# Optimization experiments

Measured on AMD Instinct MI355X. Metric: run time of the kernel, lower is better.

The kernel has to match this reference:

```python
import jax, jax.numpy as jnp
import numpy as np


def _lstm_cell(x_t, h, c, w_ih, w_hh, b):
    # x_t, h, c: [B, 1]; w_ih, w_hh: [4, 1]; b: [4]
    # PyTorch gate order: input, forget, cell(g), output
    gates = x_t @ w_ih.T + h @ w_hh.T + b  # [B, 4]
    i, f, g, o = jnp.split(gates, 4, axis=-1)
    i = jax.nn.sigmoid(i)
    f = jax.nn.sigmoid(f)
    o = jax.nn.sigmoid(o)
    g = jnp.tanh(g)
    c = f * c + i * g
    h = o * jnp.tanh(c)
    return h, c


def setup_inputs() -> dict:
    key = jax.random.key(0)
    ks = jax.random.split(key, 8)
    B, T_IN, STEPS = 32768, 1024, 512
    return {
        "x": jax.random.normal(ks[0], (B, 1, T_IN), dtype=jnp.float32),
        "t": jax.random.normal(ks[1], (B, 1, STEPS), dtype=jnp.float32),
        "h0": jax.random.normal(ks[2], (B, 1), dtype=jnp.float32),
        "c0": jax.random.normal(ks[3], (B, 1), dtype=jnp.float32),
        "w_ih": jax.random.normal(ks[4], (4, 1), dtype=jnp.float32),
        "w_hh": jax.random.normal(ks[5], (4, 1), dtype=jnp.float32),
        "b_ih": jax.random.normal(ks[6], (4,), dtype=jnp.float32) * 0.1,
        "b_hh": jax.random.normal(ks[7], (4,), dtype=jnp.float32) * 0.1,
    }


def reference(x, t, h0, c0, w_ih, w_hh, b_ih, b_hh):
    b = b_ih + b_hh
    # open loop: feed every input timestep through the LSTM cell
    xs = jnp.transpose(x[:, 0, :], (1, 0))[:, :, None]  # [T_in, B, 1]

    def open_step(carry, x_t):
        h, c = carry
        h, c = _lstm_cell(x_t, h, c, w_ih, w_hh, b)
        return (h, c), None

    (h, c), _ = jax.lax.scan(open_step, (h0, c0), xs)

    ts = jnp.transpose(t[:, 0, :], (1, 0))[:, :, None]  # [steps, B, 1]

    def closed_step(carry, _):
        h, c, x_in = carry
        h, c = _lstm_cell(x_in, h, c, w_ih, w_hh, b)
        return (h, c, h), h

    steps = ts.shape[0]
    _, preds = jax.lax.scan(closed_step, (h, c, xs[-1]), None, length=steps)
    # criterion = MSELoss(mean), accumulated per step:
    # sum_t mean_B((pred_t - t_t)^2)
    loss = jnp.sum(jnp.mean((preds - ts) ** 2, axis=(1, 2)))
    # pred_seq is detached numpy in the original -> stop_gradient here
    pred_seq = jax.lax.stop_gradient(jnp.transpose(preds[:, :, 0], (1, 0)))  # [B, steps]
    return loss, pred_seq
```

## Files before the change

### kernel.cpp

```cpp
#include <hip/hip_runtime.h>


#define L2E 1.44269504088896340736f
#define B_TOT 32768
#define T_IN 1024
#define STEPS 512
#define CPB 32
#define CH 64
#define PAD 65

__device__ __forceinline__ float ex2(float x){ return __builtin_amdgcn_exp2f(x); }
__device__ __forceinline__ float rcp(float x){ return __builtin_amdgcn_rcpf(x); }
__device__ __forceinline__ float dpp_swap1(float v){
    return __int_as_float(__builtin_amdgcn_mov_dpp(__float_as_int(v), 0xB1, 0xF, 0xF, true));
}

struct LaneK { float A1,B1,C1, A2,B2,C2, W1,W2; };

__device__ __forceinline__ void finish_step(float z1, float z2, bool odd,
                                            float& h, float& C){
    float e1 = ex2(z1);
    float e2 = ex2(z2);
    float r1 = rcp(1.0f + e1);
    float r2 = rcp(1.0f + e2);
    float s1 = dpp_swap1(r1);
    float s2 = dpp_swap1(r2);
    float ri = odd ? s1 : r1;
    float rf = odd ? r1 : s1;
    float rg = odd ? s2 : r2;
    float ro = odd ? r2 : s2;
    float g2  = fmaf(rg, -4.0f * L2E, 2.0f * L2E);
    float rfC = rf * C;
    C = fmaf(ri, g2, rfC);
    float rc = rcp(1.0f + ex2(C));
    float u  = rc + rc;
    h = fmaf(-u, ro, ro);
}

__device__ __forceinline__ void stage_issue32(const float* __restrict__ base,
                                              int row_stride, int col0, int lane,
                                              float4* v){
    const int r_lo = lane >> 4, c4 = lane & 15;
    #pragma unroll
    for (int j = 0; j < 8; ++j)
        v[j] = *(const float4*)(base + (size_t)(j*4 + r_lo) * row_stride + col0 + c4*4);
}
__device__ __forceinline__ void stage_write32(float* __restrict__ lds, int lane,
                                              const float4* v){
    const int r_lo = lane >> 4, c4 = lane & 15;
    #pragma unroll
    for (int j = 0; j < 8; ++j){
        float* p = lds + (j*4 + r_lo) * PAD + c4*4;
        p[0]=v[j].x; p[1]=v[j].y; p[2]=v[j].z; p[3]=v[j].w;
    }
}

__global__ __launch_bounds__(64) void lstm_chain_kernel(
    const float* __restrict__ x, const float* __restrict__ t,
    const float* __restrict__ h0, const float* __restrict__ c0,
    const float* __restrict__ w_ih, const float* __restrict__ w_hh,
    const float* __restrict__ b_ih, const float* __restrict__ b_hh,
    float* __restrict__ out)
{
    __shared__ float sb[2][CPB * PAD];
    __shared__ float pb[CPB * PAD];

    const int lane = threadIdx.x;
    const bool odd = lane & 1;
    const int ch   = lane >> 1;
    const int b0   = blockIdx.x * CPB;

    LaneK K;
    {
        float bi = b_ih[0] + b_hh[0], bf = b_ih[1] + b_hh[1];
        float bg = b_ih[2] + b_hh[2], bo = b_ih[3] + b_hh[3];
        float Ai = -L2E*w_ih[0], Bi = -L2E*w_hh[0], Ci = -L2E*bi;
        float Af = -L2E*w_ih[1], Bf = -L2E*w_hh[1], Cf = -L2E*bf;
        float Ag = 2.0f*L2E*w_ih[2], Bg = 2.0f*L2E*w_hh[2], Cg = 2.0f*L2E*bg;
        float Ao = -L2E*w_ih[3], Bo = -L2E*w_hh[3], Co = -L2E*bo;
        K.A1 = odd ? Af : Ai;  K.B1 = odd ? Bf : Bi;  K.C1 = odd ? Cf : Ci;
        K.A2 = odd ? Ao : Ag;  K.B2 = odd ? Bo : Bg;  K.C2 = odd ? Co : Cg;
        K.W1 = K.A1 + K.B1;    K.W2 = K.A2 + K.B2;
    }

    float h = h0[b0 + ch];
    float C = (2.0f * L2E) * c0[b0 + ch];

    const float* xbase = x + (size_t)b0 * T_IN;
    const float* tbase = t + (size_t)b0 * STEPS;

    { float4 stg[8]; stage_issue32(xbase, T_IN, 0, lane, stg); stage_write32(sb[0], lane, stg); }
    #pragma unroll 1
    for (int k = 0; k < T_IN / CH; ++k){
        float4 stg[8];
        if (k < T_IN/CH - 1) stage_issue32(xbase, T_IN, (k+1)*CH, lane, stg);
        const float* xrow = &sb[k & 1][ch * PAD];
        #pragma unroll 4
        for (int s = 0; s < CH; ++s){
            float xv = xrow[s];
            float z1 = fmaf(xv, K.A1, fmaf(h, K.B1, K.C1));
            float z2 = fmaf(xv, K.A2, fmaf(h, K.B2, K.C2));
            finish_step(z1, z2, odd, h, C);
        }
        if (k < T_IN/CH - 1) stage_write32(sb[(k+1) & 1], lane, stg);
    }
    float xin = sb[(T_IN/CH - 1) & 1][ch * PAD + (CH - 1)];

    { float4 stg[8]; stage_issue32(tbase, STEPS, 0, lane, stg); stage_write32(sb[0], lane, stg); }
    float lacc = 0.0f;

    auto cstep = [&](int s, const float* trow, float* prow){
        float z1 = fmaf(h, K.W1, K.C1);
        float z2 = fmaf(h, K.W2, K.C2);
        finish_step(z1, z2, odd, h, C);
        float d = h - trow[s];
        lacc = fmaf(d, d, lacc);
        prow[s] = h;
    };

    #pragma unroll 1
    for (int k = 0; k < STEPS / CH; ++k){
        float4 stg[8];
        if (k < STEPS/CH - 1) stage_issue32(tbase, STEPS, (k+1)*CH, lane, stg);
        const float* trow = &sb[k & 1][ch * PAD];
        float* prow = &pb[ch * PAD];
        if (k == 0){
            float z1 = fmaf(xin, K.A1, fmaf(h, K.B1, K.C1));
            float z2 = fmaf(xin, K.A2, fmaf(h, K.B2, K.C2));
            finish_step(z1, z2, odd, h, C);
            float d = h - trow[0];
            lacc = fmaf(d, d, lacc);
            prow[0] = h;
            #pragma unroll 4
            for (int s = 1; s < CH; ++s) cstep(s, trow, prow);
        } else {
            #pragma unroll 4
            for (int s = 0; s < CH; ++s) cstep(s, trow, prow);
        }
        float* obase = out + 1 + (size_t)b0 * STEPS + k * CH;
        #pragma unroll 4
        for (int r = 0; r < CPB; ++r)
            obase[(size_t)r * STEPS + lane] = pb[r * PAD + lane];
        if (k < STEPS/CH - 1) stage_write32(sb[(k+1) & 1], lane, stg);
    }

    #pragma unroll
    for (int off = 32; off > 0; off >>= 1)
        lacc += __shfl_down(lacc, off, 64);
    if (lane == 0)
        atomicAdd(out, lacc * (0.5f / (float)B_TOT));
}

extern "C" void kernel_launch(void* const* d_in, const int* in_sizes, int n_in,
                              void* d_out, int out_size, void* d_ws, size_t ws_size,
                              hipStream_t stream) {
    const float* x    = (const float*)d_in[0];
    const float* t    = (const float*)d_in[1];
    const float* h0   = (const float*)d_in[2];
    const float* c0   = (const float*)d_in[3];
    const float* w_ih = (const float*)d_in[4];
    const float* w_hh = (const float*)d_in[5];
    const float* b_ih = (const float*)d_in[6];
    const float* b_hh = (const float*)d_in[7];
    float* out = (float*)d_out;

    hipMemsetAsync(out, 0, sizeof(float), stream);

    lstm_chain_kernel<<<B_TOT / CPB, 64, 0, stream>>>(
        x, t, h0, c0, w_ih, w_hh, b_ih, b_hh, out);
}
```

Baseline: 331.1 us.

## Split LSTM gates across four lanes per chain with quad DPP broadcasts

Each batch chain now uses four lanes, one per gate, where it previously used two lanes each holding two gates. Each lane does a single exp/rcp for its gate and the four gate values are broadcast within the quad through DPP quad_perm. This shortens the per-step dependent instruction chain, at the cost of halving the chains per wave and doubling the number of blocks. The input-projection FMAs are hoisted off the recurrence, staging now uses vectorized float4 LDS reads and writes, and __syncthreads barriers plus a rescaled loss factor are added to match the new lane mapping.

```diff
diff --git a/kernel.cpp b/kernel.cpp
--- a/kernel.cpp
+++ b/kernel.cpp
@@ -5,54 +5,44 @@
 #define B_TOT 32768
 #define T_IN 1024
 #define STEPS 512
-#define CPB 32
+#define CPB 16
 #define CH 64
-#define PAD 65
+#define PAD 68
 
 __device__ __forceinline__ float ex2(float x){ return __builtin_amdgcn_exp2f(x); }
 __device__ __forceinline__ float rcp(float x){ return __builtin_amdgcn_rcpf(x); }
-__device__ __forceinline__ float dpp_swap1(float v){
-    return __int_as_float(__builtin_amdgcn_mov_dpp(__float_as_int(v), 0xB1, 0xF, 0xF, true));
+
+template<int CTRL>
+__device__ __forceinline__ float qperm(float v){
+    return __int_as_float(__builtin_amdgcn_mov_dpp(__float_as_int(v), CTRL, 0xF, 0xF, true));
 }
 
-struct LaneK { float A1,B1,C1, A2,B2,C2, W1,W2; };
-
-__device__ __forceinline__ void finish_step(float z1, float z2, bool odd,
-                                            float& h, float& C){
-    float e1 = ex2(z1);
-    float e2 = ex2(z2);
-    float r1 = rcp(1.0f + e1);
-    float r2 = rcp(1.0f + e2);
-    float s1 = dpp_swap1(r1);
-    float s2 = dpp_swap1(r2);
-    float ri = odd ? s1 : r1;
-    float rf = odd ? r1 : s1;
-    float rg = odd ? s2 : r2;
-    float ro = odd ? r2 : s2;
-    float g2  = fmaf(rg, -4.0f * L2E, 2.0f * L2E);
-    float rfC = rf * C;
-    C = fmaf(ri, g2, rfC);
+__device__ __forceinline__ void lstm_tail(float z, float& h, float& C){
+    float r  = rcp(1.0f + ex2(z));
+    float ri = qperm<0x00>(r);
+    float rf = qperm<0x55>(r);
+    float rg = qperm<0xAA>(r);
+    float ro = qperm<0xFF>(r);
+    float g2 = fmaf(rg, -4.0f * L2E, 2.0f * L2E);
+    C = fmaf(rf, C, ri * g2);
     float rc = rcp(1.0f + ex2(C));
     float u  = rc + rc;
     h = fmaf(-u, ro, ro);
 }
 
-__device__ __forceinline__ void stage_issue32(const float* __restrict__ base,
-                                              int row_stride, int col0, int lane,
-                                              float4* v){
+__device__ __forceinline__ void stage_issue16(const float* __restrict__ base,
+                                              int rs, int col0, int lane, float4* v){
     const int r_lo = lane >> 4, c4 = lane & 15;
     #pragma unroll
-    for (int j = 0; j < 8; ++j)
-        v[j] = *(const float4*)(base + (size_t)(j*4 + r_lo) * row_stride + col0 + c4*4);
+    for (int j = 0; j < 4; ++j)
+        v[j] = *(const float4*)(base + (size_t)(j*4 + r_lo) * rs + col0 + c4*4);
 }
-__device__ __forceinline__ void stage_write32(float* __restrict__ lds, int lane,
+__device__ __forceinline__ void stage_write16(float* __restrict__ lds, int lane,
                                               const float4* v){
     const int r_lo = lane >> 4, c4 = lane & 15;
     #pragma unroll
-    for (int j = 0; j < 8; ++j){
-        float* p = lds + (j*4 + r_lo) * PAD + c4*4;
-        p[0]=v[j].x; p[1]=v[j].y; p[2]=v[j].z; p[3]=v[j].w;
-    }
+    for (int j = 0; j < 4; ++j)
+        *(float4*)(lds + (j*4 + r_lo) * PAD + c4*4) = v[j];
 }
 
 __global__ __launch_bounds__(64) void lstm_chain_kernel(
@@ -66,22 +56,15 @@
     __shared__ float pb[CPB * PAD];
 
     const int lane = threadIdx.x;
-    const bool odd = lane & 1;
-    const int ch   = lane >> 1;
+    const int g    = lane & 3;
+    const int ch   = lane >> 2;
     const int b0   = blockIdx.x * CPB;
 
-    LaneK K;
-    {
-        float bi = b_ih[0] + b_hh[0], bf = b_ih[1] + b_hh[1];
-        float bg = b_ih[2] + b_hh[2], bo = b_ih[3] + b_hh[3];
-        float Ai = -L2E*w_ih[0], Bi = -L2E*w_hh[0], Ci = -L2E*bi;
-        float Af = -L2E*w_ih[1], Bf = -L2E*w_hh[1], Cf = -L2E*bf;
-        float Ag = 2.0f*L2E*w_ih[2], Bg = 2.0f*L2E*w_hh[2], Cg = 2.0f*L2E*bg;
-        float Ao = -L2E*w_ih[3], Bo = -L2E*w_hh[3], Co = -L2E*bo;
-        K.A1 = odd ? Af : Ai;  K.B1 = odd ? Bf : Bi;  K.C1 = odd ? Cf : Ci;
-        K.A2 = odd ? Ao : Ag;  K.B2 = odd ? Bo : Bg;  K.C2 = odd ? Co : Cg;
-        K.W1 = K.A1 + K.B1;    K.W2 = K.A2 + K.B2;
-    }
+    float sc = (g == 2) ? (2.0f * L2E) : (-L2E);
+    float A  = sc * w_ih[g];
+    float Bh = sc * w_hh[g];
+    float Cb = sc * (b_ih[g] + b_hh[g]);
+    float W  = A + Bh;
 
     float h = h0[b0 + ch];
     float C = (2.0f * L2E) * c0[b0 + ch];
@@ -89,66 +72,68 @@
     const float* xbase = x + (size_t)b0 * T_IN;
     const float* tbase = t + (size_t)b0 * STEPS;
 
-    { float4 stg[8]; stage_issue32(xbase, T_IN, 0, lane, stg); stage_write32(sb[0], lane, stg); }
+    { float4 stg[4]; stage_issue16(xbase, T_IN, 0, lane, stg); stage_write16(sb[0], lane, stg); }
     #pragma unroll 1
     for (int k = 0; k < T_IN / CH; ++k){
-        float4 stg[8];
-        if (k < T_IN/CH - 1) stage_issue32(xbase, T_IN, (k+1)*CH, lane, stg);
-        const float* xrow = &sb[k & 1][ch * PAD];
+        float4 stg[4];
+        if (k < T_IN/CH - 1) stage_issue16(xbase, T_IN, (k+1)*CH, lane, stg);
+        __syncthreads();
+        const float4* xrow = (const float4*)(&sb[k & 1][ch * PAD]);
         #pragma unroll 4
-        for (int s = 0; s < CH; ++s){
-            float xv = xrow[s];
-            float z1 = fmaf(xv, K.A1, fmaf(h, K.B1, K.C1));
-            float z2 = fmaf(xv, K.A2, fmaf(h, K.B2, K.C2));
-            finish_step(z1, z2, odd, h, C);
+        for (int s4 = 0; s4 < CH/4; ++s4){
+            float4 xq = xrow[s4];
+            float zx0 = fmaf(xq.x, A, Cb);
+            float zx1 = fmaf(xq.y, A, Cb);
+            float zx2 = fmaf(xq.z, A, Cb);
+            float zx3 = fmaf(xq.w, A, Cb);
+            lstm_tail(fmaf(h, Bh, zx0), h, C);
+            lstm_tail(fmaf(h, Bh, zx1), h, C);
+            lstm_tail(fmaf(h, Bh, zx2), h, C);
+            lstm_tail(fmaf(h, Bh, zx3), h, C);
         }
-        if (k < T_IN/CH - 1) stage_write32(sb[(k+1) & 1], lane, stg);
+        if (k < T_IN/CH - 1) stage_write16(sb[(k+1) & 1], lane, stg);
     }
     float xin = sb[(T_IN/CH - 1) & 1][ch * PAD + (CH - 1)];
 
-    { float4 stg[8]; stage_issue32(tbase, STEPS, 0, lane, stg); stage_write32(sb[0], lane, stg); }
+    { float4 stg[4]; stage_issue16(tbase, STEPS, 0, lane, stg); stage_write16(sb[0], lane, stg); }
     float lacc = 0.0f;
-
-    auto cstep = [&](int s, const float* trow, float* prow){
-        float z1 = fmaf(h, K.W1, K.C1);
-        float z2 = fmaf(h, K.W2, K.C2);
-        finish_step(z1, z2, odd, h, C);
-        float d = h - trow[s];
-        lacc = fmaf(d, d, lacc);
-        prow[s] = h;
-    };
-
     #pragma unroll 1
     for (int k = 0; k < STEPS / CH; ++k){
-        float4 stg[8];
-        if (k < STEPS/CH - 1) stage_issue32(tbase, STEPS, (k+1)*CH, lane, stg);
-        const float* trow = &sb[k & 1][ch * PAD];
-        float* prow = &pb[ch * PAD];
-        if (k == 0){
-            float z1 = fmaf(xin, K.A1, fmaf(h, K.B1, K.C1));
-            float z2 = fmaf(xin, K.A2, fmaf(h, K.B2, K.C2));
-            finish_step(z1, z2, odd, h, C);
-            float d = h - trow[0];
-            lacc = fmaf(d, d, lacc);
-            prow[0] = h;
-            #pragma unroll 4
-            for (int s = 1; s < CH; ++s) cstep(s, trow, prow);
-        } else {
-            #pragma unroll 4
-            for (int s = 0; s < CH; ++s) cstep(s, trow, prow);
+        float4 stg[4];
+        if (k < STEPS/CH - 1) stage_issue16(tbase, STEPS, (k+1)*CH, lane, stg);
+        __syncthreads();
+        const float4* trow = (const float4*)(&sb[k & 1][ch * PAD]);
+        #pragma unroll 2
+        for (int s4 = 0; s4 < CH/4; ++s4){
+            float4 tq = trow[s4];
+            float p0, p1, p2, p3, d;
+            if (k == 0 && s4 == 0)
+                lstm_tail(fmaf(xin, A, fmaf(h, Bh, Cb)), h, C);
+            else
+                lstm_tail(fmaf(h, W, Cb), h, C);
+            p0 = h; d = h - tq.x; lacc = fmaf(d, d, lacc);
+            lstm_tail(fmaf(h, W, Cb), h, C);
+            p1 = h; d = h - tq.y; lacc = fmaf(d, d, lacc);
+            lstm_tail(fmaf(h, W, Cb), h, C);
+            p2 = h; d = h - tq.z; lacc = fmaf(d, d, lacc);
+            lstm_tail(fmaf(h, W, Cb), h, C);
+            p3 = h; d = h - tq.w; lacc = fmaf(d, d, lacc);
+            if (g == 0)
+                *(float4*)(&pb[ch * PAD + s4 * 4]) = make_float4(p0, p1, p2, p3);
         }
+        __syncthreads();
         float* obase = out + 1 + (size_t)b0 * STEPS + k * CH;
         #pragma unroll 4
         for (int r = 0; r < CPB; ++r)
             obase[(size_t)r * STEPS + lane] = pb[r * PAD + lane];
-        if (k < STEPS/CH - 1) stage_write32(sb[(k+1) & 1], lane, stg);
+        if (k < STEPS/CH - 1) stage_write16(sb[(k+1) & 1], lane, stg);
     }
 
     #pragma unroll
     for (int off = 32; off > 0; off >>= 1)
         lacc += __shfl_down(lacc, off, 64);
     if (lane == 0)
-        atomicAdd(out, lacc * (0.5f / (float)B_TOT));
+        atomicAdd(out, lacc * (0.25f / (float)B_TOT));
 }
 
 extern "C" void kernel_launch(void* const* d_in, const int* in_sizes, int n_in,
```

After: 357.0 us. 7.8% more time.

## Shorten LSTM recurrence critical path and move loss out of the step loop

Applied to the files above, without the earlier changes.

Gate exchange between lane pairs now uses quad-permute DPP broadcasts, so the per-lane odd/even selects disappear from the serial dependency chain. The cell tail is reordered so the input term is computed off the h dependency and ro*2 is ready before the final rcp. The squared-error loss accumulation moves out of the per-step loop into the coalesced output write-back pass, reading targets from LDS. Because each element is now counted once instead of twice per lane pair, the scale changes from 0.5/B to 1/B. Unroll factors are raised to 8.

```diff
diff --git a/kernel.cpp b/kernel.cpp
--- a/kernel.cpp
+++ b/kernel.cpp
@@ -11,39 +11,34 @@
 
 __device__ __forceinline__ float ex2(float x){ return __builtin_amdgcn_exp2f(x); }
 __device__ __forceinline__ float rcp(float x){ return __builtin_amdgcn_rcpf(x); }
-__device__ __forceinline__ float dpp_swap1(float v){
-    return __int_as_float(__builtin_amdgcn_mov_dpp(__float_as_int(v), 0xB1, 0xF, 0xF, true));
+template<int CTRL>
+__device__ __forceinline__ float qp(float v){
+    return __int_as_float(__builtin_amdgcn_mov_dpp(__float_as_int(v), CTRL, 0xF, 0xF, true));
 }
 
 struct LaneK { float A1,B1,C1, A2,B2,C2, W1,W2; };
 
-__device__ __forceinline__ void finish_step(float z1, float z2, bool odd,
-                                            float& h, float& C){
-    float e1 = ex2(z1);
-    float e2 = ex2(z2);
-    float r1 = rcp(1.0f + e1);
-    float r2 = rcp(1.0f + e2);
-    float s1 = dpp_swap1(r1);
-    float s2 = dpp_swap1(r2);
-    float ri = odd ? s1 : r1;
-    float rf = odd ? r1 : s1;
-    float rg = odd ? s2 : r2;
-    float ro = odd ? r2 : s2;
-    float g2  = fmaf(rg, -4.0f * L2E, 2.0f * L2E);
-    float rfC = rf * C;
-    C = fmaf(ri, g2, rfC);
-    float rc = rcp(1.0f + ex2(C));
-    float u  = rc + rc;
-    h = fmaf(-u, ro, ro);
+__device__ __forceinline__ void tail(float z1, float z2, float& h, float& C){
+    float r1 = rcp(1.0f + ex2(z1));
+    float r2 = rcp(1.0f + ex2(z2));
+    float ri = qp<0xA0>(r1);
+    float rf = qp<0xF5>(r1);
+    float rg = qp<0xA0>(r2);
+    float ro = qp<0xF5>(r2);
+    float g2 = fmaf(rg, -4.0f * L2E, 2.0f * L2E);
+    C = fmaf(rf, C, ri * g2);
+    float e   = ex2(C);
+    float ro2 = ro + ro;
+    float rc  = rcp(1.0f + e);
+    h = fmaf(-rc, ro2, ro);
 }
 
 __device__ __forceinline__ void stage_issue32(const float* __restrict__ base,
-                                              int row_stride, int col0, int lane,
-                                              float4* v){
+                                              int rs, int col0, int lane, float4* v){
     const int r_lo = lane >> 4, c4 = lane & 15;
     #pragma unroll
     for (int j = 0; j < 8; ++j)
-        v[j] = *(const float4*)(base + (size_t)(j*4 + r_lo) * row_stride + col0 + c4*4);
+        v[j] = *(const float4*)(base + (size_t)(j*4 + r_lo) * rs + col0 + c4*4);
 }
 __device__ __forceinline__ void stage_write32(float* __restrict__ lds, int lane,
                                               const float4* v){
@@ -95,52 +90,50 @@
         float4 stg[8];
         if (k < T_IN/CH - 1) stage_issue32(xbase, T_IN, (k+1)*CH, lane, stg);
         const float* xrow = &sb[k & 1][ch * PAD];
-        #pragma unroll 4
+        #pragma unroll 8
         for (int s = 0; s < CH; ++s){
             float xv = xrow[s];
-            float z1 = fmaf(xv, K.A1, fmaf(h, K.B1, K.C1));
-            float z2 = fmaf(xv, K.A2, fmaf(h, K.B2, K.C2));
-            finish_step(z1, z2, odd, h, C);
+            float z1 = fmaf(h, K.B1, fmaf(xv, K.A1, K.C1));
+            float z2 = fmaf(h, K.B2, fmaf(xv, K.A2, K.C2));
+            tail(z1, z2, h, C);
         }
         if (k < T_IN/CH - 1) stage_write32(sb[(k+1) & 1], lane, stg);
     }
-    float xin = sb[(T_IN/CH - 1) & 1][ch * PAD + (CH - 1)];
+    float xin = sb[1][ch * PAD + (CH - 1)];
 
     { float4 stg[8]; stage_issue32(tbase, STEPS, 0, lane, stg); stage_write32(sb[0], lane, stg); }
     float lacc = 0.0f;
-
-    auto cstep = [&](int s, const float* trow, float* prow){
-        float z1 = fmaf(h, K.W1, K.C1);
-        float z2 = fmaf(h, K.W2, K.C2);
-        finish_step(z1, z2, odd, h, C);
-        float d = h - trow[s];
-        lacc = fmaf(d, d, lacc);
-        prow[s] = h;
-    };
-
     #pragma unroll 1
     for (int k = 0; k < STEPS / CH; ++k){
         float4 stg[8];
         if (k < STEPS/CH - 1) stage_issue32(tbase, STEPS, (k+1)*CH, lane, stg);
-        const float* trow = &sb[k & 1][ch * PAD];
         float* prow = &pb[ch * PAD];
         if (k == 0){
-            float z1 = fmaf(xin, K.A1, fmaf(h, K.B1, K.C1));
-            float z2 = fmaf(xin, K.A2, fmaf(h, K.B2, K.C2));
-            finish_step(z1, z2, odd, h, C);
-            float d = h - trow[0];
-            lacc = fmaf(d, d, lacc);
+            tail(fmaf(h, K.B1, fmaf(xin, K.A1, K.C1)),
+                 fmaf(h, K.B2, fmaf(xin, K.A2, K.C2)), h, C);
             prow[0] = h;
-            #pragma unroll 4
-            for (int s = 1; s < CH; ++s) cstep(s, trow, prow);
+            #pragma unroll 8
+            for (int s = 1; s < CH; ++s){
+                tail(fmaf(h, K.W1, K.C1), fmaf(h, K.W2, K.C2), h, C);
+                prow[s] = h;
+            }
         } else {
-            #pragma unroll 4
-            for (int s = 0; s < CH; ++s) cstep(s, trow, prow);
+            #pragma unroll 8
+            for (int s = 0; s < CH; ++s){
+                tail(fmaf(h, K.W1, K.C1), fmaf(h, K.W2, K.C2), h, C);
+                prow[s] = h;
+            }
         }
+        const float* trow = &sb[k & 1][0];
         float* obase = out + 1 + (size_t)b0 * STEPS + k * CH;
         #pragma unroll 4
-        for (int r = 0; r < CPB; ++r)
-            obase[(size_t)r * STEPS + lane] = pb[r * PAD + lane];
+        for (int r = 0; r < CPB; ++r){
+            float p  = pb[r * PAD + lane];
+            float tv = trow[r * PAD + lane];
+            float d  = p - tv;
+            lacc = fmaf(d, d, lacc);
+            obase[(size_t)r * STEPS + lane] = p;
+        }
         if (k < STEPS/CH - 1) stage_write32(sb[(k+1) & 1], lane, stg);
     }
 
@@ -148,7 +141,7 @@
     for (int off = 32; off > 0; off >>= 1)
         lacc += __shfl_down(lacc, off, 64);
     if (lane == 0)
-        atomicAdd(out, lacc * (0.5f / (float)B_TOT));
+        atomicAdd(out, lacc * (1.0f / (float)B_TOT));
 }
 
 extern "C" void kernel_launch(void* const* d_in, const int* in_sizes, int n_in,
```

Measured after the change: 316.8 us. 4.3% less time.
